# Kernel optimization log

Hardware: AMD Instinct MI355X
Metric: run time of the kernel (lower is better)

Reference implementation:

```python
import jax, jax.numpy as jnp
import numpy as np

B, S, D = 8, 2048, 512

def setup_inputs() -> dict:
    key = jax.random.key(0)
    k1, k2, k3 = jax.random.split(key, 3)
    context = jax.random.normal(k1, (B, S, D), dtype=jnp.float32)
    # nn.Linear default init ~ U(-1/sqrt(D), 1/sqrt(D)); scale keeps softmax sane
    bound = 1.0 / np.sqrt(D)
    W_in = jax.random.uniform(k2, (D, D), dtype=jnp.float32, minval=-bound, maxval=bound)
    W_out = jax.random.uniform(k3, (D, D), dtype=jnp.float32, minval=-bound, maxval=bound)
    return {"context": context, "W_in": W_in, "W_out": W_out}

def reference(context, W_in, W_out):
    # linear_in: x @ W_in.T (torch Linear convention)
    c = jnp.einsum('bsd,ed->bse', context, W_in)            # [B,S,D]
    scores = jnp.einsum('bsd,btd->bst', c, c)               # [B,S,S], no 1/sqrt(d) scale
    attn = jax.nn.softmax(scores, axis=-1)                  # [B,S,S]
    ctx = jnp.einsum('bst,btd->bsd', attn, c)               # [B,S,D]
    out = jnp.einsum('bsd,ed->bse', jnp.tanh(ctx), W_out)   # linear_out
    return out, attn
```

## Files before the change

### kernel.cpp

```cpp
#include <hip/hip_runtime.h>
#include <cstdint>
#include <cstddef>

#define Bc 8
#define Sc 2048
#define Dc 512

typedef float f32x4 __attribute__((ext_vector_type(4)));
typedef __bf16 bf16x8 __attribute__((ext_vector_type(8)));
typedef __bf16 bf16x4 __attribute__((ext_vector_type(4)));

__device__ __forceinline__ void gload_lds16(const void* g, void* l) {
    __builtin_amdgcn_global_load_lds((const __attribute__((address_space(1))) void*)g,
                                     (__attribute__((address_space(3))) void*)l, 16, 0, 0);
}

__device__ __forceinline__ f32x4 mfma16x16x32(bf16x8 a, bf16x8 b, f32x4 c) {
    return __builtin_amdgcn_mfma_f32_16x16x32_bf16(a, b, c, 0, 0, 0);
}

__global__ void k_convert_w(const float* __restrict__ wi, const float* __restrict__ wo,
                            __bf16* __restrict__ wib, __bf16* __restrict__ wob) {
    int i = blockIdx.x * 256 + threadIdx.x;
    wib[i] = (__bf16)wi[i];
    wob[i] = (__bf16)wo[i];
}

template <bool STATS>
__global__ __launch_bounds__(256) void k_gemm_bf16(
        const __bf16* __restrict__ A, const __bf16* __restrict__ Bt,
        float* __restrict__ C, float2* __restrict__ stats,
        int lda, int ldb, int ldc, int K,
        size_t aOffZ, size_t bOffZ, size_t cOffZ)
{
    __shared__ alignas(16) __bf16 smem[2 * 128 * 64];
    __bf16* As = smem;
    __bf16* Bs = smem + 128 * 64;
    const int tid  = threadIdx.x;
    const int wave = tid >> 6, lane = tid & 63;
    const int waveM = wave >> 1, waveN = wave & 1;
    int row0, col0, bz;
    if constexpr (STATS) {
        const int bid = blockIdx.x;
        bz   = bid & 7;
        col0 = ((bid >> 3) & 15) * 128;
        row0 = (bid >> 7) * 128;
    } else {
        bz = blockIdx.z; row0 = blockIdx.y * 128; col0 = blockIdx.x * 128;
    }
    A  += (size_t)bz * aOffZ;
    Bt += (size_t)bz * bOffZ;
    C  += (size_t)bz * cOffZ;

    f32x4 acc[4][4] = {};

    for (int k0 = 0; k0 < K; k0 += 64) {
        #pragma unroll
        for (int i = 0; i < 4; ++i) {
            int flat = i * 2048 + wave * 512 + lane * 8;
            int r  = flat >> 6;
            int cc = (flat >> 3) & 7;
            int gc = (cc ^ (r & 7)) << 3;
            gload_lds16(A  + (size_t)(row0 + r) * lda + k0 + gc, As + i * 2048 + wave * 512);
            gload_lds16(Bt + (size_t)(col0 + r) * ldb + k0 + gc, Bs + i * 2048 + wave * 512);
        }
        __syncthreads();
        #pragma unroll
        for (int ks = 0; ks < 2; ++ks) {
            const int kc = ks * 4 + (lane >> 4);
            bf16x8 av[4], bv[4];
            #pragma unroll
            for (int mi = 0; mi < 4; ++mi) {
                int r = waveM * 64 + mi * 16 + (lane & 15);
                av[mi] = *(const bf16x8*)&As[r * 64 + ((kc ^ (r & 7)) << 3)];
            }
            #pragma unroll
            for (int ni = 0; ni < 4; ++ni) {
                int r = waveN * 64 + ni * 16 + (lane & 15);
                bv[ni] = *(const bf16x8*)&Bs[r * 64 + ((kc ^ (r & 7)) << 3)];
            }
            #pragma unroll
            for (int mi = 0; mi < 4; ++mi)
                #pragma unroll
                for (int ni = 0; ni < 4; ++ni)
                    acc[mi][ni] = mfma16x16x32(av[mi], bv[ni], acc[mi][ni]);
        }
        __syncthreads();
    }

    const int rb = (lane >> 4) << 2;
    const int cb = lane & 15;
    #pragma unroll
    for (int mi = 0; mi < 4; ++mi)
        #pragma unroll
        for (int ni = 0; ni < 4; ++ni) {
            int gr = row0 + waveM * 64 + mi * 16 + rb;
            int gc = col0 + waveN * 64 + ni * 16 + cb;
            #pragma unroll
            for (int rr = 0; rr < 4; ++rr)
                C[(size_t)(gr + rr) * ldc + gc] = acc[mi][ni][rr];
        }

    if constexpr (STATS) {
        float2* sm = (float2*)smem;
        #pragma unroll
        for (int mi = 0; mi < 4; ++mi)
            #pragma unroll
            for (int rr = 0; rr < 4; ++rr) {
                float mx = fmaxf(fmaxf(acc[mi][0][rr], acc[mi][1][rr]),
                                 fmaxf(acc[mi][2][rr], acc[mi][3][rr]));
                #pragma unroll
                for (int off = 1; off < 16; off <<= 1) mx = fmaxf(mx, __shfl_xor(mx, off));
                float zs = 0.f;
                #pragma unroll
                for (int ni = 0; ni < 4; ++ni) zs += __expf(acc[mi][ni][rr] - mx);
                #pragma unroll
                for (int off = 1; off < 16; off <<= 1) zs += __shfl_xor(zs, off);
                if ((lane & 15) == 0)
                    sm[waveN * 128 + waveM * 64 + mi * 16 + rb + rr] = make_float2(mx, zs);
            }
        __syncthreads();
        if (tid < 128) {
            float2 a2 = sm[tid], b2 = sm[128 + tid];
            float M = fmaxf(a2.x, b2.x);
            float Z = a2.y * __expf(a2.x - M) + b2.y * __expf(b2.x - M);
            stats[((size_t)bz * Sc + row0 + tid) * 16 + (col0 >> 7)] = make_float2(M, Z);
        }
    }
}

__global__ __launch_bounds__(256) void k_stat_combine(const float2* __restrict__ stats,
                                                      float2* __restrict__ rowstat) {
    int r = blockIdx.x * 256 + threadIdx.x;
    float2 s[16];
    #pragma unroll
    for (int i = 0; i < 16; ++i) s[i] = stats[(size_t)r * 16 + i];
    float M = s[0].x;
    #pragma unroll
    for (int i = 1; i < 16; ++i) M = fmaxf(M, s[i].x);
    float Z = 0.f;
    #pragma unroll
    for (int i = 0; i < 16; ++i) Z += s[i].y * __expf(s[i].x - M);
    rowstat[r] = make_float2(M, 1.f / Z);
}

__global__ __launch_bounds__(512, 4) void k_pv_fused(
        float* __restrict__ attn,
        const __bf16* __restrict__ cT,
        const float2* __restrict__ rowstat,
        __bf16* __restrict__ ctx)
{
    __shared__ alignas(16) __bf16 As[32 * 64];
    __shared__ alignas(16) __bf16 Bs[512 * 64];
    const int tid  = threadIdx.x;
    const int wave = tid >> 6, lane = tid & 63;
    const int b    = blockIdx.x & 7;
    const int row0 = (blockIdx.x >> 3) * 32;
    float* sc = attn + (size_t)b * Sc * Sc;
    const __bf16* Bt = cT + (size_t)b * Dc * Sc;

    const int ar = tid >> 4;
    const int ac = (tid & 15) * 4;
    const float2 st = rowstat[b * Sc + row0 + ar];
    const float m_row = st.x, zinv = st.y;
    const int c8a  = ac >> 3;
    const int aoff = ar * 64 + ((c8a ^ (ar & 7)) << 3) + (ac & 4);

    f32x4 acc[2][4] = {};

    f32x4 s = *(const f32x4*)&sc[(size_t)(row0 + ar) * Sc + ac];

    for (int kt = 0; kt < Sc; kt += 64) {
        #pragma unroll
        for (int i = 0; i < 8; ++i) {
            int chunk = i * 512 + wave * 64 + lane;
            int r  = chunk >> 3;
            int cc = chunk & 7;
            gload_lds16(Bt + (size_t)r * Sc + kt + ((cc ^ (r & 7)) << 3),
                        Bs + (size_t)(i * 512 + wave * 64) * 8);
        }
        f32x4 p;
        #pragma unroll
        for (int j = 0; j < 4; ++j) p[j] = __expf(s[j] - m_row) * zinv;
        bf16x4 pb;
        #pragma unroll
        for (int j = 0; j < 4; ++j) pb[j] = (__bf16)p[j];
        *(bf16x4*)&As[aoff] = pb;
        __syncthreads();
        *(f32x4*)&sc[(size_t)(row0 + ar) * Sc + kt + ac] = p;
        if (kt + 64 < Sc)
            s = *(const f32x4*)&sc[(size_t)(row0 + ar) * Sc + kt + 64 + ac];
        #pragma unroll
        for (int ks = 0; ks < 2; ++ks) {
            const int kc = ks * 4 + (lane >> 4);
            bf16x8 av[2], bv[4];
            #pragma unroll
            for (int mi = 0; mi < 2; ++mi) {
                int r = mi * 16 + (lane & 15);
                av[mi] = *(const bf16x8*)&As[r * 64 + ((kc ^ (r & 7)) << 3)];
            }
            #pragma unroll
            for (int ni = 0; ni < 4; ++ni) {
                int r = wave * 64 + ni * 16 + (lane & 15);
                bv[ni] = *(const bf16x8*)&Bs[r * 64 + ((kc ^ (r & 7)) << 3)];
            }
            #pragma unroll
            for (int mi = 0; mi < 2; ++mi)
                #pragma unroll
                for (int ni = 0; ni < 4; ++ni)
                    acc[mi][ni] = mfma16x16x32(av[mi], bv[ni], acc[mi][ni]);
        }
        __syncthreads();
    }

    const int rb = (lane >> 4) << 2;
    const int cb = lane & 15;
    #pragma unroll
    for (int mi = 0; mi < 2; ++mi)
        #pragma unroll
        for (int ni = 0; ni < 4; ++ni) {
            int gr = row0 + mi * 16 + rb;
            int gc = wave * 64 + ni * 16 + cb;
            #pragma unroll
            for (int rr = 0; rr < 4; ++rr)
                ctx[(size_t)(b * Sc + gr + rr) * Dc + gc] = (__bf16)tanhf(acc[mi][ni][rr]);
        }
}

__global__ __launch_bounds__(256) void k_cproj(
        const float* __restrict__ A, const __bf16* __restrict__ Bt,
        __bf16* __restrict__ Cb, __bf16* __restrict__ CTb)
{
    __shared__ alignas(16) char smem[49152];
    float*  Asf = (float*)smem;
    __bf16* Bs  = (__bf16*)(smem + 32768);
    const int tid  = threadIdx.x;
    const int wave = tid >> 6, lane = tid & 63;
    const int waveM = wave >> 1, waveN = wave & 1;
    const int row0 = blockIdx.y * 128;
    const int col0 = blockIdx.x * 128;

    f32x4 acc[4][4] = {};

    for (int k0 = 0; k0 < Dc; k0 += 64) {
        #pragma unroll
        for (int i = 0; i < 8; ++i) {
            int flat = i * 1024 + wave * 256 + lane * 4;
            int r  = flat >> 6;
            int cc = (flat >> 2) & 15;
            int gc = (cc ^ (r & 15)) << 2;
            gload_lds16(A + (size_t)(row0 + r) * Dc + k0 + gc, Asf + i * 1024 + wave * 256);
        }
        #pragma unroll
        for (int i = 0; i < 4; ++i) {
            int flat = i * 2048 + wave * 512 + lane * 8;
            int r  = flat >> 6;
            int cc = (flat >> 3) & 7;
            int gc = (cc ^ (r & 7)) << 3;
            gload_lds16(Bt + (size_t)(col0 + r) * Dc + k0 + gc, Bs + i * 2048 + wave * 512);
        }
        __syncthreads();
        #pragma unroll
        for (int ks = 0; ks < 2; ++ks) {
            const int kc8 = ks * 4 + (lane >> 4);
            const int kc4 = kc8 << 1;
            bf16x8 av[4], bv[4];
            #pragma unroll
            for (int mi = 0; mi < 4; ++mi) {
                int r  = waveM * 64 + mi * 16 + (lane & 15);
                int r4 = r & 15;
                f32x4 lo = *(const f32x4*)&Asf[r * 64 + (((kc4    ) ^ r4) << 2)];
                f32x4 hi = *(const f32x4*)&Asf[r * 64 + (((kc4 + 1) ^ r4) << 2)];
                bf16x8 a;
                a[0] = (__bf16)lo[0]; a[1] = (__bf16)lo[1]; a[2] = (__bf16)lo[2]; a[3] = (__bf16)lo[3];
                a[4] = (__bf16)hi[0]; a[5] = (__bf16)hi[1]; a[6] = (__bf16)hi[2]; a[7] = (__bf16)hi[3];
                av[mi] = a;
            }
            #pragma unroll
            for (int ni = 0; ni < 4; ++ni) {
                int r = waveN * 64 + ni * 16 + (lane & 15);
                bv[ni] = *(const bf16x8*)&Bs[r * 64 + ((kc8 ^ (r & 7)) << 3)];
            }
            #pragma unroll
            for (int mi = 0; mi < 4; ++mi)
                #pragma unroll
                for (int ni = 0; ni < 4; ++ni)
                    acc[mi][ni] = mfma16x16x32(av[mi], bv[ni], acc[mi][ni]);
        }
        __syncthreads();
    }

    const int rb = (lane >> 4) << 2;
    const int cb = lane & 15;
    __bf16* T = (__bf16*)smem;
    #pragma unroll
    for (int mi = 0; mi < 4; ++mi)
        #pragma unroll
        for (int ni = 0; ni < 4; ++ni) {
            int lr = waveM * 64 + mi * 16 + rb;
            int lc = waveN * 64 + ni * 16 + cb;
            #pragma unroll
            for (int rr = 0; rr < 4; ++rr) {
                __bf16 h = (__bf16)acc[mi][ni][rr];
                Cb[(size_t)(row0 + lr + rr) * Dc + col0 + lc] = h;
                T[lc * 136 + lr + rr] = h;
            }
        }
    __syncthreads();
    const int bb = row0 >> 11;
    const int s0 = row0 & 2047;
    #pragma unroll
    for (int i = 0; i < 8; ++i) {
        int n  = i * 16 + (tid >> 4);
        int mo = (tid & 15) * 8;
        bf16x8 v = *(const bf16x8*)&T[n * 136 + mo];
        *(bf16x8*)&CTb[(size_t)bb * Dc * Sc + (size_t)(col0 + n) * Sc + s0 + mo] = v;
    }
}

extern "C" void kernel_launch(void* const* d_in, const int* in_sizes, int n_in,
                              void* d_out, int out_size, void* d_ws, size_t ws_size,
                              hipStream_t stream)
{
    (void)in_sizes; (void)n_in; (void)out_size; (void)ws_size;
    const float* context = (const float*)d_in[0];
    const float* W_in    = (const float*)d_in[1];
    const float* W_out   = (const float*)d_in[2];
    float* out  = (float*)d_out;
    float* attn = out + (size_t)Bc * Sc * Dc;

    char* ws = (char*)d_ws;
    __bf16* c_bf    = (__bf16*)ws;
    __bf16* cT_bf   = (__bf16*)(ws + 16777216);
    __bf16* wi_bf   = (__bf16*)(ws + 33554432);
    __bf16* wo_bf   = (__bf16*)(ws + 34078720);
    float2* stats   = (float2*)(ws + 34603008);
    float2* rowstat = (float2*)(ws + 36700160);

    k_convert_w<<<dim3(Dc * Dc / 256), 256, 0, stream>>>(W_in, W_out, wi_bf, wo_bf);

    k_cproj<<<dim3(Dc / 128, (Bc * Sc) / 128), 256, 0, stream>>>(context, wi_bf, c_bf, cT_bf);

    k_gemm_bf16<true><<<dim3(Bc * 16 * 16), 256, 0, stream>>>(
        c_bf, c_bf, attn, stats, Dc, Dc, Sc, Dc,
        (size_t)Sc * Dc, (size_t)Sc * Dc, (size_t)Sc * Sc);

    k_stat_combine<<<dim3(Bc * Sc / 256), 256, 0, stream>>>(stats, rowstat);

    k_pv_fused<<<dim3((Sc / 32) * Bc), 512, 0, stream>>>(attn, cT_bf, rowstat, c_bf);

    k_gemm_bf16<false><<<dim3(Dc / 128, (Bc * Sc) / 128, 1), 256, 0, stream>>>(
        c_bf, wo_bf, out, nullptr, Dc, Dc, Dc, Dc, 0, 0, 0);
}
```

Measured before the change: 191.5 us.

## Double-buffer PV kernel LDS tiles and double the row tile

Restructures the fused softmax-normalize and P·V kernel so each block handles 64 rows instead of 32, with a K step of 32 and double-buffered A/B shared-memory tiles. The next tile's probabilities and B loads are issued before the current tile's MFMAs, leaving one barrier per iteration. The aim is to overlap global-to-LDS transfers with compute and to reuse each B tile across twice as many rows. In exchange the grid shrinks to 256 blocks, the accumulators double, and the launch-bounds occupancy hint is dropped, which may reduce occupancy.

Result: slower. 201.3 us (+5.1%).

```diff
diff --git a/kernel.cpp b/kernel.cpp
--- a/kernel.cpp
+++ b/kernel.cpp
@@ -144,79 +144,98 @@
     rowstat[r] = make_float2(M, 1.f / Z);
 }
 
-__global__ __launch_bounds__(512, 4) void k_pv_fused(
+__global__ __launch_bounds__(512) void k_pv_fused(
         float* __restrict__ attn,
         const __bf16* __restrict__ cT,
         const float2* __restrict__ rowstat,
         __bf16* __restrict__ ctx)
 {
-    __shared__ alignas(16) __bf16 As[32 * 64];
-    __shared__ alignas(16) __bf16 Bs[512 * 64];
+    __shared__ alignas(16) __bf16 As[2][64 * 32];
+    __shared__ alignas(16) __bf16 Bs[2][512 * 32];
     const int tid  = threadIdx.x;
     const int wave = tid >> 6, lane = tid & 63;
     const int b    = blockIdx.x & 7;
-    const int row0 = (blockIdx.x >> 3) * 32;
+    const int row0 = (blockIdx.x >> 3) * 64;
     float* sc = attn + (size_t)b * Sc * Sc;
     const __bf16* Bt = cT + (size_t)b * Dc * Sc;
 
-    const int ar = tid >> 4;
-    const int ac = (tid & 15) * 4;
+    const int ar = tid >> 3;
+    const int ac = (tid & 7) * 4;
     const float2 st = rowstat[b * Sc + row0 + ar];
     const float m_row = st.x, zinv = st.y;
-    const int c8a  = ac >> 3;
-    const int aoff = ar * 64 + ((c8a ^ (ar & 7)) << 3) + (ac & 4);
-
-    f32x4 acc[2][4] = {};
-
-    f32x4 s = *(const f32x4*)&sc[(size_t)(row0 + ar) * Sc + ac];
-
-    for (int kt = 0; kt < Sc; kt += 64) {
-        #pragma unroll
-        for (int i = 0; i < 8; ++i) {
+    const int a_addr = ar * 32 + (((ac >> 3) ^ (ar & 3)) << 3) + (ac & 7);
+    float* srow = sc + (size_t)(row0 + ar) * Sc + ac;
+
+    f32x4 acc[4][4] = {};
+
+    auto stageB = [&](int buf, int kt) {
+        #pragma unroll
+        for (int i = 0; i < 4; ++i) {
             int chunk = i * 512 + wave * 64 + lane;
-            int r  = chunk >> 3;
-            int cc = chunk & 7;
-            gload_lds16(Bt + (size_t)r * Sc + kt + ((cc ^ (r & 7)) << 3),
-                        Bs + (size_t)(i * 512 + wave * 64) * 8);
-        }
-        f32x4 p;
-        #pragma unroll
-        for (int j = 0; j < 4; ++j) p[j] = __expf(s[j] - m_row) * zinv;
+            int r  = chunk >> 2;
+            int cc = chunk & 3;
+            gload_lds16(Bt + (size_t)r * Sc + kt + ((cc ^ (r & 3)) << 3),
+                        &Bs[buf][(i * 512 + wave * 64) * 8]);
+        }
+    };
+
+    const int NT = Sc / 32;
+
+    f32x4 s_next = *(const f32x4*)&srow[0];
+    f32x4 p;
+    #pragma unroll
+    for (int j = 0; j < 4; ++j) p[j] = __expf(s_next[j] - m_row) * zinv;
+    {
         bf16x4 pb;
         #pragma unroll
         for (int j = 0; j < 4; ++j) pb[j] = (__bf16)p[j];
-        *(bf16x4*)&As[aoff] = pb;
-        __syncthreads();
-        *(f32x4*)&sc[(size_t)(row0 + ar) * Sc + kt + ac] = p;
-        if (kt + 64 < Sc)
-            s = *(const f32x4*)&sc[(size_t)(row0 + ar) * Sc + kt + 64 + ac];
-        #pragma unroll
-        for (int ks = 0; ks < 2; ++ks) {
-            const int kc = ks * 4 + (lane >> 4);
-            bf16x8 av[2], bv[4];
-            #pragma unroll
-            for (int mi = 0; mi < 2; ++mi) {
-                int r = mi * 16 + (lane & 15);
-                av[mi] = *(const bf16x8*)&As[r * 64 + ((kc ^ (r & 7)) << 3)];
-            }
-            #pragma unroll
-            for (int ni = 0; ni < 4; ++ni) {
-                int r = wave * 64 + ni * 16 + (lane & 15);
-                bv[ni] = *(const bf16x8*)&Bs[r * 64 + ((kc ^ (r & 7)) << 3)];
-            }
-            #pragma unroll
-            for (int mi = 0; mi < 2; ++mi)
-                #pragma unroll
-                for (int ni = 0; ni < 4; ++ni)
-                    acc[mi][ni] = mfma16x16x32(av[mi], bv[ni], acc[mi][ni]);
-        }
+        *(bf16x4*)&As[0][a_addr] = pb;
+    }
+    stageB(0, 0);
+    s_next = *(const f32x4*)&srow[32];
+    __syncthreads();
+
+    for (int t = 0; t < NT; ++t) {
+        const int cur = t & 1;
+        if (t + 1 < NT) {
+            f32x4 pn;
+            #pragma unroll
+            for (int j = 0; j < 4; ++j) pn[j] = __expf(s_next[j] - m_row) * zinv;
+            bf16x4 pb;
+            #pragma unroll
+            for (int j = 0; j < 4; ++j) pb[j] = (__bf16)pn[j];
+            *(bf16x4*)&As[cur ^ 1][a_addr] = pb;
+            stageB(cur ^ 1, (t + 1) * 32);
+            *(f32x4*)&srow[t * 32] = p;
+            if (t + 2 < NT) s_next = *(const f32x4*)&srow[(t + 2) * 32];
+            p = pn;
+        } else {
+            *(f32x4*)&srow[t * 32] = p;
+        }
+        const int kc = lane >> 4;
+        bf16x8 av[4], bv[4];
+        #pragma unroll
+        for (int mi = 0; mi < 4; ++mi) {
+            int r = mi * 16 + (lane & 15);
+            av[mi] = *(const bf16x8*)&As[cur][r * 32 + ((kc ^ (r & 3)) << 3)];
+        }
+        #pragma unroll
+        for (int ni = 0; ni < 4; ++ni) {
+            int r = wave * 64 + ni * 16 + (lane & 15);
+            bv[ni] = *(const bf16x8*)&Bs[cur][r * 32 + ((kc ^ (r & 3)) << 3)];
+        }
+        #pragma unroll
+        for (int mi = 0; mi < 4; ++mi)
+            #pragma unroll
+            for (int ni = 0; ni < 4; ++ni)
+                acc[mi][ni] = mfma16x16x32(av[mi], bv[ni], acc[mi][ni]);
         __syncthreads();
     }
 
     const int rb = (lane >> 4) << 2;
     const int cb = lane & 15;
     #pragma unroll
-    for (int mi = 0; mi < 2; ++mi)
+    for (int mi = 0; mi < 4; ++mi)
         #pragma unroll
         for (int ni = 0; ni < 4; ++ni) {
             int gr = row0 + mi * 16 + rb;
@@ -347,7 +366,7 @@
 
     k_stat_combine<<<dim3(Bc * Sc / 256), 256, 0, stream>>>(stats, rowstat);
 
-    k_pv_fused<<<dim3((Sc / 32) * Bc), 512, 0, stream>>>(attn, cT_bf, rowstat, c_bf);
+    k_pv_fused<<<dim3((Sc / 64) * Bc), 512, 0, stream>>>(attn, cT_bf, rowstat, c_bf);
 
     k_gemm_bf16<false><<<dim3(Dc / 128, (Bc * Sc) / 128, 1), 256, 0, stream>>>(
         c_bf, wo_bf, out, nullptr, Dc, Dc, Dc, Dc, 0, 0, 0);
```

## Software-pipeline attn normalization and ctx GEMM loads with manual waitcnt barriers

Applied to the files above, without the earlier changes.

Restructures the P@V loop so all LDS fragments for a tile are read into registers first, then the next tile's B async loads, exp/normalize and prob write-back are issued before the MFMAs run. Explicit s_waitcnt with vmcnt counts and raw s_barrier replace __syncthreads, so global loads can overlap the MFMA work. This relies on the hand-set vmcnt counts being correct. It also raises register pressure from holding both k-slices of fragments at once.

New measurement: 198.2 us. +3.5%, slower.

```diff
diff --git a/kernel.cpp b/kernel.cpp
--- a/kernel.cpp
+++ b/kernel.cpp
@@ -163,54 +163,94 @@
     const int ac = (tid & 15) * 4;
     const float2 st = rowstat[b * Sc + row0 + ar];
     const float m_row = st.x, zinv = st.y;
-    const int c8a  = ac >> 3;
-    const int aoff = ar * 64 + ((c8a ^ (ar & 7)) << 3) + (ac & 4);
+    const int a_addr = ar * 64 + (((ac >> 3) ^ (ar & 7)) << 3) + (ac & 4);
+    float* srow = sc + (size_t)(row0 + ar) * Sc + ac;
 
     f32x4 acc[2][4] = {};
-
-    f32x4 s = *(const f32x4*)&sc[(size_t)(row0 + ar) * Sc + ac];
-
-    for (int kt = 0; kt < Sc; kt += 64) {
+    const int NT = Sc / 64;
+
+    auto stageB = [&](int kt) {
         #pragma unroll
         for (int i = 0; i < 8; ++i) {
             int chunk = i * 512 + wave * 64 + lane;
             int r  = chunk >> 3;
             int cc = chunk & 7;
             gload_lds16(Bt + (size_t)r * Sc + kt + ((cc ^ (r & 7)) << 3),
-                        Bs + (size_t)(i * 512 + wave * 64) * 8);
-        }
-        f32x4 p;
-        #pragma unroll
-        for (int j = 0; j < 4; ++j) p[j] = __expf(s[j] - m_row) * zinv;
+                        Bs + (size_t)chunk * 8);
+        }
+    };
+
+    f32x4 s_cur = *(const f32x4*)&srow[0];
+    f32x4 p_cur;
+    #pragma unroll
+    for (int j = 0; j < 4; ++j) p_cur[j] = __expf(s_cur[j] - m_row) * zinv;
+    {
         bf16x4 pb;
         #pragma unroll
-        for (int j = 0; j < 4; ++j) pb[j] = (__bf16)p[j];
-        *(bf16x4*)&As[aoff] = pb;
-        __syncthreads();
-        *(f32x4*)&sc[(size_t)(row0 + ar) * Sc + kt + ac] = p;
-        if (kt + 64 < Sc)
-            s = *(const f32x4*)&sc[(size_t)(row0 + ar) * Sc + kt + 64 + ac];
+        for (int j = 0; j < 4; ++j) pb[j] = (__bf16)p_cur[j];
+        *(bf16x4*)&As[a_addr] = pb;
+    }
+    stageB(0);
+    __builtin_amdgcn_sched_barrier(0);
+    f32x4 s_next = *(const f32x4*)&srow[64];
+    asm volatile("s_waitcnt vmcnt(1) lgkmcnt(0)" ::: "memory");
+    __builtin_amdgcn_sched_barrier(0);
+    __builtin_amdgcn_s_barrier();
+
+    for (int t = 0; t < NT; ++t) {
+        bf16x8 av[2][2], bv[2][4];
         #pragma unroll
         for (int ks = 0; ks < 2; ++ks) {
             const int kc = ks * 4 + (lane >> 4);
-            bf16x8 av[2], bv[4];
             #pragma unroll
             for (int mi = 0; mi < 2; ++mi) {
                 int r = mi * 16 + (lane & 15);
-                av[mi] = *(const bf16x8*)&As[r * 64 + ((kc ^ (r & 7)) << 3)];
+                av[mi][ks] = *(const bf16x8*)&As[r * 64 + ((kc ^ (r & 7)) << 3)];
             }
             #pragma unroll
             for (int ni = 0; ni < 4; ++ni) {
                 int r = wave * 64 + ni * 16 + (lane & 15);
-                bv[ni] = *(const bf16x8*)&Bs[r * 64 + ((kc ^ (r & 7)) << 3)];
-            }
+                bv[ks][ni] = *(const bf16x8*)&Bs[r * 64 + ((kc ^ (r & 7)) << 3)];
+            }
+        }
+        asm volatile("s_waitcnt lgkmcnt(0)" ::: "memory");
+        __builtin_amdgcn_sched_barrier(0);
+        __builtin_amdgcn_s_barrier();
+
+        if (t + 1 < NT) {
+            stageB((t + 1) * 64);
+            __builtin_amdgcn_sched_barrier(0);
+            f32x4 p_next;
+            #pragma unroll
+            for (int j = 0; j < 4; ++j) p_next[j] = __expf(s_next[j] - m_row) * zinv;
+            bf16x4 pb;
+            #pragma unroll
+            for (int j = 0; j < 4; ++j) pb[j] = (__bf16)p_next[j];
+            *(bf16x4*)&As[a_addr] = pb;
+            *(f32x4*)&srow[t * 64] = p_cur;
+            if (t + 2 < NT)
+                s_next = *(const f32x4*)&srow[(t + 2) * 64];
+            p_cur = p_next;
+        } else {
+            *(f32x4*)&srow[t * 64] = p_cur;
+        }
+
+        #pragma unroll
+        for (int ks = 0; ks < 2; ++ks)
             #pragma unroll
             for (int mi = 0; mi < 2; ++mi)
                 #pragma unroll
                 for (int ni = 0; ni < 4; ++ni)
-                    acc[mi][ni] = mfma16x16x32(av[mi], bv[ni], acc[mi][ni]);
-        }
-        __syncthreads();
+                    acc[mi][ni] = mfma16x16x32(av[mi][ks], bv[ks][ni], acc[mi][ni]);
+
+        if (t + 1 < NT) {
+            if (t + 2 < NT)
+                asm volatile("s_waitcnt vmcnt(2) lgkmcnt(0)" ::: "memory");
+            else
+                asm volatile("s_waitcnt vmcnt(1) lgkmcnt(0)" ::: "memory");
+            __builtin_amdgcn_sched_barrier(0);
+            __builtin_amdgcn_s_barrier();
+        }
     }
 
     const int rb = (lane >> 4) << 2;
```

## Store bf16 partial exponentials from scores kernel and rescale in PV pass

Applied to the files above, without the earlier changes.

The scores kernel now computes exp(s - local max) per 64-column tile, writes it as bf16 to a workspace buffer, and emits local max/sum stats. A combine kernel builds a per-tile correction factor, and the PV kernel multiplies the bf16 exponentials by it instead of re-reading fp32 scores and recomputing exp. This cuts the fp32 score write plus read round trip through attn to a half-size bf16 round trip. The exchange is reduced precision in the returned attention probabilities and extra workspace.

Measured after the change: 189.7 us. No clear change (-1.0%).

```diff
diff --git a/kernel.cpp b/kernel.cpp
--- a/kernel.cpp
+++ b/kernel.cpp
@@ -26,43 +26,33 @@
     wob[i] = (__bf16)wo[i];
 }
 
-template <bool STATS>
-__global__ __launch_bounds__(256) void k_gemm_bf16(
-        const __bf16* __restrict__ A, const __bf16* __restrict__ Bt,
-        float* __restrict__ C, float2* __restrict__ stats,
-        int lda, int ldb, int ldc, int K,
-        size_t aOffZ, size_t bOffZ, size_t cOffZ)
+__global__ __launch_bounds__(256) void k_scores(
+        const __bf16* __restrict__ c, __bf16* __restrict__ Ebuf,
+        float2* __restrict__ stats)
 {
-    __shared__ alignas(16) __bf16 smem[2 * 128 * 64];
-    __bf16* As = smem;
-    __bf16* Bs = smem + 128 * 64;
+    __shared__ alignas(16) char smem[34816];
+    __bf16* As = (__bf16*)smem;
+    __bf16* Bs = (__bf16*)(smem + 16384);
     const int tid  = threadIdx.x;
     const int wave = tid >> 6, lane = tid & 63;
     const int waveM = wave >> 1, waveN = wave & 1;
-    int row0, col0, bz;
-    if constexpr (STATS) {
-        const int bid = blockIdx.x;
-        bz   = bid & 7;
-        col0 = ((bid >> 3) & 15) * 128;
-        row0 = (bid >> 7) * 128;
-    } else {
-        bz = blockIdx.z; row0 = blockIdx.y * 128; col0 = blockIdx.x * 128;
-    }
-    A  += (size_t)bz * aOffZ;
-    Bt += (size_t)bz * bOffZ;
-    C  += (size_t)bz * cOffZ;
+    const int bid  = blockIdx.x;
+    const int bz   = bid & 7;
+    const int col0 = ((bid >> 3) & 15) * 128;
+    const int row0 = (bid >> 7) * 128;
+    const __bf16* A  = c + (size_t)bz * Sc * Dc;
 
     f32x4 acc[4][4] = {};
 
-    for (int k0 = 0; k0 < K; k0 += 64) {
+    for (int k0 = 0; k0 < Dc; k0 += 64) {
         #pragma unroll
         for (int i = 0; i < 4; ++i) {
             int flat = i * 2048 + wave * 512 + lane * 8;
             int r  = flat >> 6;
             int cc = (flat >> 3) & 7;
             int gc = (cc ^ (r & 7)) << 3;
-            gload_lds16(A  + (size_t)(row0 + r) * lda + k0 + gc, As + i * 2048 + wave * 512);
-            gload_lds16(Bt + (size_t)(col0 + r) * ldb + k0 + gc, Bs + i * 2048 + wave * 512);
+            gload_lds16(A + (size_t)(row0 + r) * Dc + k0 + gc, As + i * 2048 + wave * 512);
+            gload_lds16(A + (size_t)(col0 + r) * Dc + k0 + gc, Bs + i * 2048 + wave * 512);
         }
         __syncthreads();
         #pragma unroll
@@ -90,64 +80,61 @@
 
     const int rb = (lane >> 4) << 2;
     const int cb = lane & 15;
+    __bf16* Es = (__bf16*)smem;
     #pragma unroll
     for (int mi = 0; mi < 4; ++mi)
         #pragma unroll
-        for (int ni = 0; ni < 4; ++ni) {
-            int gr = row0 + waveM * 64 + mi * 16 + rb;
-            int gc = col0 + waveN * 64 + ni * 16 + cb;
-            #pragma unroll
-            for (int rr = 0; rr < 4; ++rr)
-                C[(size_t)(gr + rr) * ldc + gc] = acc[mi][ni][rr];
-        }
-
-    if constexpr (STATS) {
-        float2* sm = (float2*)smem;
-        #pragma unroll
-        for (int mi = 0; mi < 4; ++mi)
-            #pragma unroll
-            for (int rr = 0; rr < 4; ++rr) {
-                float mx = fmaxf(fmaxf(acc[mi][0][rr], acc[mi][1][rr]),
-                                 fmaxf(acc[mi][2][rr], acc[mi][3][rr]));
-                #pragma unroll
-                for (int off = 1; off < 16; off <<= 1) mx = fmaxf(mx, __shfl_xor(mx, off));
-                float zs = 0.f;
-                #pragma unroll
-                for (int ni = 0; ni < 4; ++ni) zs += __expf(acc[mi][ni][rr] - mx);
-                #pragma unroll
-                for (int off = 1; off < 16; off <<= 1) zs += __shfl_xor(zs, off);
-                if ((lane & 15) == 0)
-                    sm[waveN * 128 + waveM * 64 + mi * 16 + rb + rr] = make_float2(mx, zs);
-            }
-        __syncthreads();
-        if (tid < 128) {
-            float2 a2 = sm[tid], b2 = sm[128 + tid];
-            float M = fmaxf(a2.x, b2.x);
-            float Z = a2.y * __expf(a2.x - M) + b2.y * __expf(b2.x - M);
-            stats[((size_t)bz * Sc + row0 + tid) * 16 + (col0 >> 7)] = make_float2(M, Z);
-        }
-    }
-}
-
-__global__ __launch_bounds__(256) void k_stat_combine(const float2* __restrict__ stats,
-                                                      float2* __restrict__ rowstat) {
+        for (int rr = 0; rr < 4; ++rr) {
+            float mx = fmaxf(fmaxf(acc[mi][0][rr], acc[mi][1][rr]),
+                             fmaxf(acc[mi][2][rr], acc[mi][3][rr]));
+            #pragma unroll
+            for (int off = 1; off < 16; off <<= 1) mx = fmaxf(mx, __shfl_xor(mx, off));
+            const int rloc = waveM * 64 + mi * 16 + rb + rr;
+            float zs = 0.f;
+            #pragma unroll
+            for (int ni = 0; ni < 4; ++ni) {
+                float e = __expf(acc[mi][ni][rr] - mx);
+                zs += e;
+                Es[rloc * 136 + waveN * 64 + ni * 16 + cb] = (__bf16)e;
+            }
+            #pragma unroll
+            for (int off = 1; off < 16; off <<= 1) zs += __shfl_xor(zs, off);
+            if ((lane & 15) == 0)
+                stats[((size_t)bz * Sc + row0 + rloc) * 32 + (col0 >> 6) + waveN] =
+                    make_float2(mx, zs);
+        }
+    __syncthreads();
+    #pragma unroll
+    for (int p = 0; p < 8; ++p) {
+        int r  = p * 16 + (tid >> 4);
+        int cc = (tid & 15) * 8;
+        bf16x8 v = *(const bf16x8*)&Es[r * 136 + cc];
+        *(bf16x8*)&Ebuf[((size_t)bz * Sc + row0 + r) * Sc + col0 + cc] = v;
+    }
+}
+
+__global__ __launch_bounds__(256) void k_combine(const float2* __restrict__ stats,
+                                                 float* __restrict__ corrTab) {
     int r = blockIdx.x * 256 + threadIdx.x;
-    float2 s[16];
-    #pragma unroll
-    for (int i = 0; i < 16; ++i) s[i] = stats[(size_t)r * 16 + i];
+    float2 s[32];
+    #pragma unroll
+    for (int i = 0; i < 32; ++i) s[i] = stats[(size_t)r * 32 + i];
     float M = s[0].x;
     #pragma unroll
-    for (int i = 1; i < 16; ++i) M = fmaxf(M, s[i].x);
+    for (int i = 1; i < 32; ++i) M = fmaxf(M, s[i].x);
     float Z = 0.f;
     #pragma unroll
-    for (int i = 0; i < 16; ++i) Z += s[i].y * __expf(s[i].x - M);
-    rowstat[r] = make_float2(M, 1.f / Z);
+    for (int i = 0; i < 32; ++i) Z += s[i].y * __expf(s[i].x - M);
+    float zi = 1.f / Z;
+    #pragma unroll
+    for (int i = 0; i < 32; ++i) corrTab[(size_t)r * 32 + i] = __expf(s[i].x - M) * zi;
 }
 
 __global__ __launch_bounds__(512, 4) void k_pv_fused(
+        const __bf16* __restrict__ Buf,
+        const __bf16* __restrict__ cT,
+        const float* __restrict__ corrTab,
         float* __restrict__ attn,
-        const __bf16* __restrict__ cT,
-        const float2* __restrict__ rowstat,
         __bf16* __restrict__ ctx)
 {
     __shared__ alignas(16) __bf16 As[32 * 64];
@@ -156,43 +143,51 @@
     const int wave = tid >> 6, lane = tid & 63;
     const int b    = blockIdx.x & 7;
     const int row0 = (blockIdx.x >> 3) * 32;
-    float* sc = attn + (size_t)b * Sc * Sc;
     const __bf16* Bt = cT + (size_t)b * Dc * Sc;
 
     const int ar = tid >> 4;
     const int ac = (tid & 15) * 4;
-    const float2 st = rowstat[b * Sc + row0 + ar];
-    const float m_row = st.x, zinv = st.y;
-    const int c8a  = ac >> 3;
-    const int aoff = ar * 64 + ((c8a ^ (ar & 7)) << 3) + (ac & 4);
+    const __bf16* erow = Buf + ((size_t)b * Sc + row0 + ar) * Sc + ac;
+    const float*  crow = corrTab + ((size_t)b * Sc + row0 + ar) * 32;
+    float*        prow = attn + ((size_t)b * Sc + row0 + ar) * Sc + ac;
+    const int a_addr = ar * 64 + (((ac >> 3) ^ (ar & 7)) << 3) + (ac & 4);
 
     f32x4 acc[2][4] = {};
-
-    f32x4 s = *(const f32x4*)&sc[(size_t)(row0 + ar) * Sc + ac];
-
-    for (int kt = 0; kt < Sc; kt += 64) {
+    const int NT = Sc / 64;
+
+    auto stageB = [&](int kt) {
         #pragma unroll
         for (int i = 0; i < 8; ++i) {
             int chunk = i * 512 + wave * 64 + lane;
             int r  = chunk >> 3;
             int cc = chunk & 7;
             gload_lds16(Bt + (size_t)r * Sc + kt + ((cc ^ (r & 7)) << 3),
-                        Bs + (size_t)(i * 512 + wave * 64) * 8);
-        }
+                        Bs + (size_t)chunk * 8);
+        }
+    };
+
+    bf16x4 e_cur = *(const bf16x4*)&erow[0];
+    float  c_cur = crow[0];
+
+    for (int t = 0; t < NT; ++t) {
+        stageB(t * 64);
         f32x4 p;
         #pragma unroll
-        for (int j = 0; j < 4; ++j) p[j] = __expf(s[j] - m_row) * zinv;
+        for (int j = 0; j < 4; ++j) p[j] = (float)e_cur[j] * c_cur;
         bf16x4 pb;
         #pragma unroll
         for (int j = 0; j < 4; ++j) pb[j] = (__bf16)p[j];
-        *(bf16x4*)&As[aoff] = pb;
-        __syncthreads();
-        *(f32x4*)&sc[(size_t)(row0 + ar) * Sc + kt + ac] = p;
-        if (kt + 64 < Sc)
-            s = *(const f32x4*)&sc[(size_t)(row0 + ar) * Sc + kt + 64 + ac];
+        *(bf16x4*)&As[a_addr] = pb;
+        __syncthreads();
+        *(f32x4*)&prow[t * 64] = p;
+        if (t + 1 < NT) {
+            e_cur = *(const bf16x4*)&erow[(t + 1) * 64];
+            c_cur = crow[t + 1];
+        }
+        const int kcb = lane >> 4;
         #pragma unroll
         for (int ks = 0; ks < 2; ++ks) {
-            const int kc = ks * 4 + (lane >> 4);
+            const int kc = ks * 4 + kcb;
             bf16x8 av[2], bv[4];
             #pragma unroll
             for (int mi = 0; mi < 2; ++mi) {
@@ -224,6 +219,69 @@
             #pragma unroll
             for (int rr = 0; rr < 4; ++rr)
                 ctx[(size_t)(b * Sc + gr + rr) * Dc + gc] = (__bf16)tanhf(acc[mi][ni][rr]);
+        }
+}
+
+__global__ __launch_bounds__(256) void k_gemm_bf16(
+        const __bf16* __restrict__ A, const __bf16* __restrict__ Bt,
+        float* __restrict__ C, int lda, int ldb, int ldc, int K)
+{
+    __shared__ alignas(16) __bf16 smem[2 * 128 * 64];
+    __bf16* As = smem;
+    __bf16* Bs = smem + 128 * 64;
+    const int tid  = threadIdx.x;
+    const int wave = tid >> 6, lane = tid & 63;
+    const int waveM = wave >> 1, waveN = wave & 1;
+    const int row0 = blockIdx.y * 128;
+    const int col0 = blockIdx.x * 128;
+
+    f32x4 acc[4][4] = {};
+
+    for (int k0 = 0; k0 < K; k0 += 64) {
+        #pragma unroll
+        for (int i = 0; i < 4; ++i) {
+            int flat = i * 2048 + wave * 512 + lane * 8;
+            int r  = flat >> 6;
+            int cc = (flat >> 3) & 7;
+            int gc = (cc ^ (r & 7)) << 3;
+            gload_lds16(A  + (size_t)(row0 + r) * lda + k0 + gc, As + i * 2048 + wave * 512);
+            gload_lds16(Bt + (size_t)(col0 + r) * ldb + k0 + gc, Bs + i * 2048 + wave * 512);
+        }
+        __syncthreads();
+        #pragma unroll
+        for (int ks = 0; ks < 2; ++ks) {
+            const int kc = ks * 4 + (lane >> 4);
+            bf16x8 av[4], bv[4];
+            #pragma unroll
+            for (int mi = 0; mi < 4; ++mi) {
+                int r = waveM * 64 + mi * 16 + (lane & 15);
+                av[mi] = *(const bf16x8*)&As[r * 64 + ((kc ^ (r & 7)) << 3)];
+            }
+            #pragma unroll
+            for (int ni = 0; ni < 4; ++ni) {
+                int r = waveN * 64 + ni * 16 + (lane & 15);
+                bv[ni] = *(const bf16x8*)&Bs[r * 64 + ((kc ^ (r & 7)) << 3)];
+            }
+            #pragma unroll
+            for (int mi = 0; mi < 4; ++mi)
+                #pragma unroll
+                for (int ni = 0; ni < 4; ++ni)
+                    acc[mi][ni] = mfma16x16x32(av[mi], bv[ni], acc[mi][ni]);
+        }
+        __syncthreads();
+    }
+
+    const int rb = (lane >> 4) << 2;
+    const int cb = lane & 15;
+    #pragma unroll
+    for (int mi = 0; mi < 4; ++mi)
+        #pragma unroll
+        for (int ni = 0; ni < 4; ++ni) {
+            int gr = row0 + waveM * 64 + mi * 16 + rb;
+            int gc = col0 + waveN * 64 + ni * 16 + cb;
+            #pragma unroll
+            for (int rr = 0; rr < 4; ++rr)
+                C[(size_t)(gr + rr) * ldc + gc] = acc[mi][ni][rr];
         }
 }
 
@@ -335,20 +393,19 @@
     __bf16* wi_bf   = (__bf16*)(ws + 33554432);
     __bf16* wo_bf   = (__bf16*)(ws + 34078720);
     float2* stats   = (float2*)(ws + 34603008);
-    float2* rowstat = (float2*)(ws + 36700160);
+    float*  corrTab = (float*)(ws + 38797312);
+    __bf16* Ebuf    = (__bf16*)(ws + 40894464);
 
     k_convert_w<<<dim3(Dc * Dc / 256), 256, 0, stream>>>(W_in, W_out, wi_bf, wo_bf);
 
     k_cproj<<<dim3(Dc / 128, (Bc * Sc) / 128), 256, 0, stream>>>(context, wi_bf, c_bf, cT_bf);
 
-    k_gemm_bf16<true><<<dim3(Bc * 16 * 16), 256, 0, stream>>>(
-        c_bf, c_bf, attn, stats, Dc, Dc, Sc, Dc,
-        (size_t)Sc * Dc, (size_t)Sc * Dc, (size_t)Sc * Sc);
-
-    k_stat_combine<<<dim3(Bc * Sc / 256), 256, 0, stream>>>(stats, rowstat);
-
-    k_pv_fused<<<dim3((Sc / 32) * Bc), 512, 0, stream>>>(attn, cT_bf, rowstat, c_bf);
-
-    k_gemm_bf16<false><<<dim3(Dc / 128, (Bc * Sc) / 128, 1), 256, 0, stream>>>(
-        c_bf, wo_bf, out, nullptr, Dc, Dc, Dc, Dc, 0, 0, 0);
-}
+    k_scores<<<dim3(Bc * 16 * 16), 256, 0, stream>>>(c_bf, Ebuf, stats);
+
+    k_combine<<<dim3(Bc * Sc / 256), 256, 0, stream>>>(stats, corrTab);
+
+    k_pv_fused<<<dim3((Sc / 32) * Bc), 512, 0, stream>>>(Ebuf, cT_bf, corrTab, attn, c_bf);
+
+    k_gemm_bf16<<<dim3(Dc / 128, (Bc * Sc) / 128, 1), 256, 0, stream>>>(
+        c_bf, wo_bf, out, Dc, Dc, Dc, Dc);
+}
```
